# Kernel tuning notes

Measured on AMD Instinct MI355X. Metric: run time of the kernel, lower is better.

## Reference

```python
import jax, jax.numpy as jnp
import numpy as np


def _pad_kernel_like(kernel_oc0, H, W, ks):
    # torch: F.pad(k,(p,p,p,p)) then if shape mismatch F.pad(k,(0,1,0,1))
    p = (H - ks) // 2
    extra = H - (ks + 2 * p)  # 0 or 1
    return jnp.pad(kernel_oc0, ((0, 0), (p, p + extra), (p, p + extra)))


def setup_inputs() -> dict:
    key = jax.random.key(0)
    k1, k2 = jax.random.split(key)
    B, C, H, W = 8, 16, 128, 128
    O, KS = 32, 9
    x = jax.random.normal(k1, (B, C, H, W), dtype=jnp.float32)
    # kaiming_uniform-ish init scale
    fan_in = C * KS * KS
    bound = float(np.sqrt(6.0 / fan_in))
    kernel = jax.random.uniform(k2, (O, C, KS, KS), dtype=jnp.float32,
                                minval=-bound, maxval=bound)
    return {"x": x, "kernel": kernel}


def reference(x, kernel):
    # x: [B,C,H,W] float32, kernel: [O,C,ks,ks] float32
    B, C, H, W = x.shape
    O, ks = kernel.shape[0], kernel.shape[-1]
    # Faithful to original bug: only kernel[:, 0] is used for every input channel.
    k = _pad_kernel_like(kernel[:, 0], H, W, ks)  # [O,H,W]
    # 4f optical FFT convolution: ifftshift -> FFT -> multiply -> IFFT -> fftshift -> |.|
    Fx = jnp.fft.fft2(jnp.fft.ifftshift(x, axes=(-2, -1)))   # [B,C,H,W] complex64
    Fk = jnp.fft.fft2(jnp.fft.ifftshift(k, axes=(-2, -1)))   # [O,H,W]   complex64
    prod = Fx[:, None, :, :, :] * Fk[None, :, None, :, :]    # [B,O,C,H,W]
    field = jnp.fft.fftshift(jnp.fft.ifft2(prod), axes=(-2, -1))
    out_pc = jnp.abs(field)                                  # per-(out,in)-channel intensity
    return out_pc.sum(axis=2)                                # [B,O,H,W]
```

## Files before the change

kernel.cpp:

```cpp
#include <hip/hip_runtime.h>


typedef __attribute__((ext_vector_type(8)))  short  short8;
typedef __attribute__((ext_vector_type(4)))  float  float4v;
typedef __attribute__((ext_vector_type(4)))  unsigned int uint4v;

#define XR_ROWS 138
#define XR_RDW  72
#define XR_CH_DW (XR_ROWS * XR_RDW)
#define XR_TOT_DW (128 * XR_CH_DW)
#define BPRE_OFF ((size_t)128 * XR_ROWS * 288)
#define CHB 3168

__device__ __forceinline__ unsigned int f2bf(float f) {
    union { float f; unsigned int u; } a; a.f = f;
    unsigned int u = a.u;
    u += 0x7fffu + ((u >> 16) & 1u);
    return u >> 16;
}

#if __has_builtin(__builtin_amdgcn_alignbit)
#define ALIGN16(hi_, lo_) __builtin_amdgcn_alignbit((hi_), (lo_), 16)
#else
#define ALIGN16(hi_, lo_) \
    (unsigned int)((((unsigned long long)(hi_) << 32) | (lo_)) >> 16)
#endif

#define FRAG_EVEN(q_) __builtin_bit_cast(short8, (uint4v){                    \
        wnd[(q_)+0], wnd[(q_)+1], wnd[(q_)+2], wnd[(q_)+3]})
#define FRAG_ODD(q_)  __builtin_bit_cast(short8, (uint4v){                    \
        ALIGN16(wnd[(q_)+1], wnd[(q_)+0]),                                    \
        ALIGN16(wnd[(q_)+2], wnd[(q_)+1]),                                    \
        ALIGN16(wnd[(q_)+3], wnd[(q_)+2]),                                    \
        ALIGN16(wnd[(q_)+4], wnd[(q_)+3])})

__device__ __forceinline__ void gload_lds16(const void* g, void* l) {
    __builtin_amdgcn_global_load_lds(
        (const __attribute__((address_space(1))) unsigned int*)g,
        (__attribute__((address_space(3))) unsigned int*)l, 16, 0, 0);
}

__global__ __launch_bounds__(256)
void optical_prep_x_69698729279498(const float* __restrict__ x,
                                   unsigned int* __restrict__ xr) {
    for (int idx = blockIdx.x * 256 + threadIdx.x; idx < XR_TOT_DW;
         idx += gridDim.x * 256) {
        int bc  = idx / XR_CH_DW;
        int rem = idx - bc * XR_CH_DW;
        int r   = rem / XR_RDW;
        int ccd = rem - r * XR_RDW;
        int cc  = 2 * ccd;
        const float* xp = x + (bc << 14) + ((r & 127) << 7);
        float v0 = xp[(132 - cc) & 127];
        float v1 = xp[(131 - cc) & 127];
        xr[idx] = f2bf(v0) | (f2bf(v1) << 16);
    }
}

__global__ __launch_bounds__(64)
void optical_prep_b_69698729279498(const float* __restrict__ kern,
                                   uint4v* __restrict__ bpre) {
    const int l  = threadIdx.x;
    const int lk = l & 15;
    const int g2 = l >> 4;
    for (int oh = 0; oh < 2; ++oh) {
        const int o = oh * 16 + lk;
        for (int ck = 0; ck < 5; ++ck) {
            const int ti  = 2 * ck + (g2 >> 1);
            const int tj0 = (g2 & 1) * 8;
            unsigned int pk[4];
#pragma unroll
            for (int ee = 0; ee < 4; ++ee) {
                int tj_a = tj0 + 2 * ee, tj_b = tj_a + 1;
                float va = (ti <= 8 && tj_a <= 8) ? kern[o * 1296 + ti * 9 + tj_a] : 0.f;
                float vb = (ti <= 8 && tj_b <= 8) ? kern[o * 1296 + ti * 9 + tj_b] : 0.f;
                pk[ee] = f2bf(va) | (f2bf(vb) << 16);
            }
            bpre[(oh * 5 + ck) * 64 + l] = (uint4v){pk[0], pk[1], pk[2], pk[3]};
        }
    }
}

__global__ __launch_bounds__(512, 4)
void optical_conv_69698729279498(const unsigned int* __restrict__ xr,
                                 const uint4v* __restrict__ bpre,
                                 float* __restrict__ out) {
    __shared__ __align__(16) unsigned short ldsb[16 * (CHB / 2)];

    const int tid = threadIdx.x;
    const int l   = tid & 63;
    const int w   = tid >> 6;
    const int h   = w & 1;
    const int oh  = (w >> 1) & 1;
    const int rh  = w >> 2;
    const int i0  = blockIdx.x * 2;
    const int b   = blockIdx.y;

    const int lk   = l & 15;
    const int g    = (l >> 4) & 1;
    const int hi32 = l >> 5;
    const int g2   = l >> 4;
    const int o    = oh * 16 + lk;

    const int wstart = (i0 >= 4) ? (i0 - 4) : (i0 + 124);
    const char* xr8 = (const char*)xr;
#pragma unroll
    for (int cw = 0; cw < 2; ++cw) {
        const int ch = 2 * w + cw;
        const char* src = xr8 + ((size_t)((b * 16 + ch) * XR_ROWS + wstart)) * 288;
        char* dst = (char*)ldsb + ch * CHB;
        gload_lds16(src + 0 * 1024 + l * 16, dst + 0 * 1024);
        gload_lds16(src + 1 * 1024 + l * 16, dst + 1 * 1024);
        gload_lds16(src + 2 * 1024 + l * 16, dst + 2 * 1024);
        if (l < 6)
            gload_lds16(src + 3072 + l * 16, dst + 3072);
    }

    short8 Bf[5];
#pragma unroll
    for (int ck = 0; ck < 5; ++ck)
        Bf[ck] = __builtin_bit_cast(short8, bpre[(oh * 5 + ck) * 64 + l]);

    __syncthreads();

    float4v acc[4];
#pragma unroll
    for (int pp = 0; pp < 4; ++pp) acc[pp] = (float4v){0.f, 0.f, 0.f, 0.f};
    const float4v zero4 = (float4v){0.f, 0.f, 0.f, 0.f};

    const char* lb = (const char*)ldsb
                   + (240 - 16 * lk + 16 * g) + (1 - hi32 + rh) * 288;

    for (int c = 0; c < 16; ++c) {
        float4v D[4];
#pragma unroll
        for (int ck = 0; ck < 5; ++ck) {
            const char* p = lb + (8 - 2 * ck) * 288;
            uint4v w0 = *(const uint4v*)p;
            uint4v w1 = *(const uint4v*)(p + 16);
            unsigned int wnd[8] = {w0.x, w0.y, w0.z, w0.w, w1.x, w1.y, w1.z, w1.w};
            if (h == 0) {
                short8 f0 = FRAG_ODD(3),  f1 = FRAG_EVEN(3);
                short8 f2 = FRAG_ODD(2),  f3 = FRAG_EVEN(2);
                D[0] = __builtin_amdgcn_mfma_f32_16x16x32_bf16(f0, Bf[ck], ck ? D[0] : zero4, 0, 0, 0);
                D[1] = __builtin_amdgcn_mfma_f32_16x16x32_bf16(f1, Bf[ck], ck ? D[1] : zero4, 0, 0, 0);
                D[2] = __builtin_amdgcn_mfma_f32_16x16x32_bf16(f2, Bf[ck], ck ? D[2] : zero4, 0, 0, 0);
                D[3] = __builtin_amdgcn_mfma_f32_16x16x32_bf16(f3, Bf[ck], ck ? D[3] : zero4, 0, 0, 0);
            } else {
                short8 f0 = FRAG_ODD(1),  f1 = FRAG_EVEN(1);
                short8 f2 = FRAG_ODD(0),  f3 = FRAG_EVEN(0);
                D[0] = __builtin_amdgcn_mfma_f32_16x16x32_bf16(f0, Bf[ck], ck ? D[0] : zero4, 0, 0, 0);
                D[1] = __builtin_amdgcn_mfma_f32_16x16x32_bf16(f1, Bf[ck], ck ? D[1] : zero4, 0, 0, 0);
                D[2] = __builtin_amdgcn_mfma_f32_16x16x32_bf16(f2, Bf[ck], ck ? D[2] : zero4, 0, 0, 0);
                D[3] = __builtin_amdgcn_mfma_f32_16x16x32_bf16(f3, Bf[ck], ck ? D[3] : zero4, 0, 0, 0);
            }
        }
#pragma unroll
        for (int pp = 0; pp < 4; ++pp)
#pragma unroll
            for (int e = 0; e < 4; ++e) acc[pp][e] += fabsf(D[pp][e]);
        lb += CHB;
    }

    const int i = i0 + rh;
    float* ob = out + ((((size_t)(b * 32 + o)) * 128 + i) << 7);
#pragma unroll
    for (int pp = 0; pp < 4; ++pp) {
        const int pprime = 4 * h + pp;
#pragma unroll
        for (int e = 0; e < 4; ++e)
            ob[32 * g2 + 8 * e + pprime] = acc[pp][e];
    }
}

extern "C" void kernel_launch(void* const* d_in, const int* in_sizes, int n_in,
                              void* d_out, int out_size, void* d_ws, size_t ws_size,
                              hipStream_t stream) {
    const float* x = (const float*)d_in[0];
    const float* kern = (const float*)d_in[1];
    float* out = (float*)d_out;
    unsigned int* xr = (unsigned int*)d_ws;
    uint4v* bpre = (uint4v*)((char*)d_ws + BPRE_OFF);

    hipLaunchKernelGGL(optical_prep_x_69698729279498, dim3(4096), dim3(256),
                       0, stream, x, xr);
    hipLaunchKernelGGL(optical_prep_b_69698729279498, dim3(1), dim3(64),
                       0, stream, kern, bpre);
    hipLaunchKernelGGL(optical_conv_69698729279498, dim3(64, 8), dim3(512),
                       0, stream, xr, bpre, out);
}
```

Measured before the change: 99.55 us.

## Merge prep kernels and give each conv wave both column halves

The two preprocessing kernels are merged into one launch, with an extra block that packs the kernel weights while the other blocks convert x to bf16. The conv kernel drops from 512 to 256 threads. Each wave now computes all eight column fragments from one set of LDS loads instead of splitting them across two waves, which removes duplicate LDS reads of the shifted windows. Outputs are written as float4 vector stores. In exchange each wave holds more accumulators, so register pressure rises and fewer waves are available per block to hide latency.

```diff
diff --git a/kernel.cpp b/kernel.cpp
--- a/kernel.cpp
+++ b/kernel.cpp
@@ -11,6 +11,8 @@
 #define XR_TOT_DW (128 * XR_CH_DW)
 #define BPRE_OFF ((size_t)128 * XR_ROWS * 288)
 #define CHB 3168
+#define PREP_BLOCKS 2048
+#define PREP_STRIDE (PREP_BLOCKS * 256)
 
 __device__ __forceinline__ unsigned int f2bf(float f) {
     union { float f; unsigned int u; } a; a.f = f;
@@ -41,10 +43,36 @@
 }
 
 __global__ __launch_bounds__(256)
-void optical_prep_x_69698729279498(const float* __restrict__ x,
-                                   unsigned int* __restrict__ xr) {
+void optical_prep_69698729279498(const float* __restrict__ x,
+                                 const float* __restrict__ kern,
+                                 unsigned int* __restrict__ xr,
+                                 uint4v* __restrict__ bpre) {
+    if (blockIdx.x == PREP_BLOCKS) {
+        const int l = threadIdx.x;
+        if (l < 64) {
+            const int lk = l & 15;
+            const int g2 = l >> 4;
+            for (int oh = 0; oh < 2; ++oh) {
+                const int o = oh * 16 + lk;
+                for (int ck = 0; ck < 5; ++ck) {
+                    const int ti  = 2 * ck + (g2 >> 1);
+                    const int tj0 = (g2 & 1) * 8;
+                    unsigned int pk[4];
+#pragma unroll
+                    for (int ee = 0; ee < 4; ++ee) {
+                        int tj_a = tj0 + 2 * ee, tj_b = tj_a + 1;
+                        float va = (ti <= 8 && tj_a <= 8) ? kern[o * 1296 + ti * 9 + tj_a] : 0.f;
+                        float vb = (ti <= 8 && tj_b <= 8) ? kern[o * 1296 + ti * 9 + tj_b] : 0.f;
+                        pk[ee] = f2bf(va) | (f2bf(vb) << 16);
+                    }
+                    bpre[(oh * 5 + ck) * 64 + l] = (uint4v){pk[0], pk[1], pk[2], pk[3]};
+                }
+            }
+        }
+        return;
+    }
     for (int idx = blockIdx.x * 256 + threadIdx.x; idx < XR_TOT_DW;
-         idx += gridDim.x * 256) {
+         idx += PREP_STRIDE) {
         int bc  = idx / XR_CH_DW;
         int rem = idx - bc * XR_CH_DW;
         int r   = rem / XR_RDW;
@@ -57,31 +85,7 @@
     }
 }
 
-__global__ __launch_bounds__(64)
-void optical_prep_b_69698729279498(const float* __restrict__ kern,
-                                   uint4v* __restrict__ bpre) {
-    const int l  = threadIdx.x;
-    const int lk = l & 15;
-    const int g2 = l >> 4;
-    for (int oh = 0; oh < 2; ++oh) {
-        const int o = oh * 16 + lk;
-        for (int ck = 0; ck < 5; ++ck) {
-            const int ti  = 2 * ck + (g2 >> 1);
-            const int tj0 = (g2 & 1) * 8;
-            unsigned int pk[4];
-#pragma unroll
-            for (int ee = 0; ee < 4; ++ee) {
-                int tj_a = tj0 + 2 * ee, tj_b = tj_a + 1;
-                float va = (ti <= 8 && tj_a <= 8) ? kern[o * 1296 + ti * 9 + tj_a] : 0.f;
-                float vb = (ti <= 8 && tj_b <= 8) ? kern[o * 1296 + ti * 9 + tj_b] : 0.f;
-                pk[ee] = f2bf(va) | (f2bf(vb) << 16);
-            }
-            bpre[(oh * 5 + ck) * 64 + l] = (uint4v){pk[0], pk[1], pk[2], pk[3]};
-        }
-    }
-}
-
-__global__ __launch_bounds__(512, 4)
+__global__ __launch_bounds__(256, 2)
 void optical_conv_69698729279498(const unsigned int* __restrict__ xr,
                                  const uint4v* __restrict__ bpre,
                                  float* __restrict__ out) {
@@ -90,9 +94,8 @@
     const int tid = threadIdx.x;
     const int l   = tid & 63;
     const int w   = tid >> 6;
-    const int h   = w & 1;
-    const int oh  = (w >> 1) & 1;
-    const int rh  = w >> 2;
+    const int oh  = w & 1;
+    const int rh  = w >> 1;
     const int i0  = blockIdx.x * 2;
     const int b   = blockIdx.y;
 
@@ -105,8 +108,8 @@
     const int wstart = (i0 >= 4) ? (i0 - 4) : (i0 + 124);
     const char* xr8 = (const char*)xr;
 #pragma unroll
-    for (int cw = 0; cw < 2; ++cw) {
-        const int ch = 2 * w + cw;
+    for (int cw = 0; cw < 4; ++cw) {
+        const int ch = 4 * w + cw;
         const char* src = xr8 + ((size_t)((b * 16 + ch) * XR_ROWS + wstart)) * 288;
         char* dst = (char*)ldsb + ch * CHB;
         gload_lds16(src + 0 * 1024 + l * 16, dst + 0 * 1024);
@@ -123,53 +126,55 @@
 
     __syncthreads();
 
-    float4v acc[4];
+    float4v acc[8];
 #pragma unroll
-    for (int pp = 0; pp < 4; ++pp) acc[pp] = (float4v){0.f, 0.f, 0.f, 0.f};
+    for (int p = 0; p < 8; ++p) acc[p] = (float4v){0.f, 0.f, 0.f, 0.f};
     const float4v zero4 = (float4v){0.f, 0.f, 0.f, 0.f};
 
     const char* lb = (const char*)ldsb
                    + (240 - 16 * lk + 16 * g) + (1 - hi32 + rh) * 288;
 
     for (int c = 0; c < 16; ++c) {
-        float4v D[4];
+        uint4v wa[5], wb[5];
 #pragma unroll
         for (int ck = 0; ck < 5; ++ck) {
             const char* p = lb + (8 - 2 * ck) * 288;
-            uint4v w0 = *(const uint4v*)p;
-            uint4v w1 = *(const uint4v*)(p + 16);
-            unsigned int wnd[8] = {w0.x, w0.y, w0.z, w0.w, w1.x, w1.y, w1.z, w1.w};
-            if (h == 0) {
-                short8 f0 = FRAG_ODD(3),  f1 = FRAG_EVEN(3);
-                short8 f2 = FRAG_ODD(2),  f3 = FRAG_EVEN(2);
-                D[0] = __builtin_amdgcn_mfma_f32_16x16x32_bf16(f0, Bf[ck], ck ? D[0] : zero4, 0, 0, 0);
-                D[1] = __builtin_amdgcn_mfma_f32_16x16x32_bf16(f1, Bf[ck], ck ? D[1] : zero4, 0, 0, 0);
-                D[2] = __builtin_amdgcn_mfma_f32_16x16x32_bf16(f2, Bf[ck], ck ? D[2] : zero4, 0, 0, 0);
-                D[3] = __builtin_amdgcn_mfma_f32_16x16x32_bf16(f3, Bf[ck], ck ? D[3] : zero4, 0, 0, 0);
-            } else {
-                short8 f0 = FRAG_ODD(1),  f1 = FRAG_EVEN(1);
-                short8 f2 = FRAG_ODD(0),  f3 = FRAG_EVEN(0);
-                D[0] = __builtin_amdgcn_mfma_f32_16x16x32_bf16(f0, Bf[ck], ck ? D[0] : zero4, 0, 0, 0);
-                D[1] = __builtin_amdgcn_mfma_f32_16x16x32_bf16(f1, Bf[ck], ck ? D[1] : zero4, 0, 0, 0);
-                D[2] = __builtin_amdgcn_mfma_f32_16x16x32_bf16(f2, Bf[ck], ck ? D[2] : zero4, 0, 0, 0);
-                D[3] = __builtin_amdgcn_mfma_f32_16x16x32_bf16(f3, Bf[ck], ck ? D[3] : zero4, 0, 0, 0);
-            }
+            wa[ck] = *(const uint4v*)p;
+            wb[ck] = *(const uint4v*)(p + 16);
+        }
+        float4v D[8];
+#pragma unroll
+        for (int ck = 0; ck < 5; ++ck) {
+            unsigned int wnd[8] = {wa[ck].x, wa[ck].y, wa[ck].z, wa[ck].w,
+                                   wb[ck].x, wb[ck].y, wb[ck].z, wb[ck].w};
+            short8 f0 = FRAG_ODD(3),  f1 = FRAG_EVEN(3);
+            short8 f2 = FRAG_ODD(2),  f3 = FRAG_EVEN(2);
+            short8 f4 = FRAG_ODD(1),  f5 = FRAG_EVEN(1);
+            short8 f6 = FRAG_ODD(0),  f7 = FRAG_EVEN(0);
+            D[0] = __builtin_amdgcn_mfma_f32_16x16x32_bf16(f0, Bf[ck], ck ? D[0] : zero4, 0, 0, 0);
+            D[1] = __builtin_amdgcn_mfma_f32_16x16x32_bf16(f1, Bf[ck], ck ? D[1] : zero4, 0, 0, 0);
+            D[2] = __builtin_amdgcn_mfma_f32_16x16x32_bf16(f2, Bf[ck], ck ? D[2] : zero4, 0, 0, 0);
+            D[3] = __builtin_amdgcn_mfma_f32_16x16x32_bf16(f3, Bf[ck], ck ? D[3] : zero4, 0, 0, 0);
+            D[4] = __builtin_amdgcn_mfma_f32_16x16x32_bf16(f4, Bf[ck], ck ? D[4] : zero4, 0, 0, 0);
+            D[5] = __builtin_amdgcn_mfma_f32_16x16x32_bf16(f5, Bf[ck], ck ? D[5] : zero4, 0, 0, 0);
+            D[6] = __builtin_amdgcn_mfma_f32_16x16x32_bf16(f6, Bf[ck], ck ? D[6] : zero4, 0, 0, 0);
+            D[7] = __builtin_amdgcn_mfma_f32_16x16x32_bf16(f7, Bf[ck], ck ? D[7] : zero4, 0, 0, 0);
         }
 #pragma unroll
-        for (int pp = 0; pp < 4; ++pp)
+        for (int p = 0; p < 8; ++p)
 #pragma unroll
-            for (int e = 0; e < 4; ++e) acc[pp][e] += fabsf(D[pp][e]);
+            for (int e = 0; e < 4; ++e) acc[p][e] += fabsf(D[p][e]);
         lb += CHB;
     }
 
     const int i = i0 + rh;
     float* ob = out + ((((size_t)(b * 32 + o)) * 128 + i) << 7);
 #pragma unroll
-    for (int pp = 0; pp < 4; ++pp) {
-        const int pprime = 4 * h + pp;
-#pragma unroll
-        for (int e = 0; e < 4; ++e)
-            ob[32 * g2 + 8 * e + pprime] = acc[pp][e];
+    for (int e = 0; e < 4; ++e) {
+        float4v lo = (float4v){acc[0][e], acc[1][e], acc[2][e], acc[3][e]};
+        float4v hi = (float4v){acc[4][e], acc[5][e], acc[6][e], acc[7][e]};
+        *(float4v*)&ob[32 * g2 + 8 * e]     = lo;
+        *(float4v*)&ob[32 * g2 + 8 * e + 4] = hi;
     }
 }
 
@@ -182,10 +187,8 @@
     unsigned int* xr = (unsigned int*)d_ws;
     uint4v* bpre = (uint4v*)((char*)d_ws + BPRE_OFF);
 
-    hipLaunchKernelGGL(optical_prep_x_69698729279498, dim3(4096), dim3(256),
-                       0, stream, x, xr);
-    hipLaunchKernelGGL(optical_prep_b_69698729279498, dim3(1), dim3(64),
-                       0, stream, kern, bpre);
-    hipLaunchKernelGGL(optical_conv_69698729279498, dim3(64, 8), dim3(512),
+    hipLaunchKernelGGL(optical_prep_69698729279498, dim3(PREP_BLOCKS + 1),
+                       dim3(256), 0, stream, x, kern, xr, bpre);
+    hipLaunchKernelGGL(optical_conv_69698729279498, dim3(64, 8), dim3(256),
                        0, stream, xr, bpre, out);
 }
```

Result: faster. 94.75 us (-4.8%).
